# Optimization experiments

Measured on AMD Instinct MI355X. Metric: run time of the kernel, lower is better.

The kernel has to match this reference:

```python
import jax, jax.numpy as jnp
import numpy as np

Z, H, W = 8, 96, 192
WZ, WH, WW = 2, 6, 12
C, HEADS, DEPTH, B = 192, 6, 2, 1
NZ, NH, NW = Z // WZ, H // WH, W // WW
LW = WZ * WH * WW            # 144 tokens per window
WIN_TYPES = NZ * NH          # 64 earth-specific window types
NPOS = WZ * WZ * WH * WH * (2 * WW - 1)  # 3312 relative-position entries
HD = C // HEADS
SCALE = HD ** -0.5
SZ, SH, SW = WZ // 2, WH // 2, WW // 2


def _position_index():
    czi = np.arange(WZ); czj = -np.arange(WZ) * WZ
    chi = np.arange(WH); chj = -np.arange(WH) * WH
    cw = np.arange(WW)
    c1 = np.stack(np.meshgrid(czi, chi, cw, indexing='ij'), 0).reshape(3, -1)
    c2 = np.stack(np.meshgrid(czj, chj, cw, indexing='ij'), 0).reshape(3, -1)
    coords = (c1[:, :, None] - c2[:, None, :]).transpose(1, 2, 0).astype(np.int64).copy()
    coords[:, :, 2] += WW - 1
    coords[:, :, 1] *= 2 * WW - 1
    coords[:, :, 0] *= (2 * WW - 1) * WH * WH
    return coords.sum(-1).reshape(-1)


def _attention_mask():
    m = np.zeros((Z, H, W))
    zs = (slice(0, -WZ), slice(-WZ, -SZ), slice(-SZ, None))
    hs = (slice(0, -WH), slice(-WH, -SH), slice(-SH, None))
    ws = (slice(0, -WW), slice(-WW, -SW), slice(-SW, None))
    cnt = 0
    for z in zs:
        for h in hs:
            for w in ws:
                m[z, h, w] = cnt
                cnt += 1
    mw = m.reshape(NZ, WZ, NH, WH, NW, WW).transpose(0, 2, 4, 1, 3, 5).reshape(-1, LW)
    d = mw[:, None, :] - mw[:, :, None]
    return np.where(d != 0, -100.0, 0.0).astype(np.float32)


def setup_inputs() -> dict:
    key = jax.random.key(0)
    ks = jax.random.split(key, 12)
    s = 0.02
    def rn(k, shape):
        return jax.random.normal(k, shape, jnp.float32) * s
    return {
        'x': jax.random.normal(ks[0], (B, Z * H * W, C), jnp.float32),
        'qkv_w': rn(ks[1], (DEPTH, C, 3 * C)),
        'qkv_b': rn(ks[2], (DEPTH, 3 * C)),
        'proj_w': rn(ks[3], (DEPTH, C, C)),
        'proj_b': rn(ks[4], (DEPTH, C)),
        'bias_tab': rn(ks[5], (DEPTH, NPOS, WIN_TYPES, HEADS)),
        'n1_g': jnp.ones((DEPTH, C), jnp.float32),
        'n1_b': jnp.zeros((DEPTH, C), jnp.float32),
        'n2_g': jnp.ones((DEPTH, C), jnp.float32),
        'n2_b': jnp.zeros((DEPTH, C), jnp.float32),
        'mlp_w1': rn(ks[6], (DEPTH, C, 4 * C)),
        'mlp_b1': rn(ks[7], (DEPTH, 4 * C)),
        'mlp_w2': rn(ks[8], (DEPTH, 4 * C, C)),
        'mlp_b2': rn(ks[9], (DEPTH, C)),
        'pos_index': jnp.asarray(_position_index(), jnp.int32),
        'attn_mask': jnp.asarray(_attention_mask()),
    }


def _ln(x, g, b):
    m = x.mean(-1, keepdims=True)
    v = jnp.mean((x - m) ** 2, -1, keepdims=True)
    return (x - m) / jnp.sqrt(v + 1e-5) * g + b


def _forward(x, qkv_w, qkv_b, proj_w, proj_b, bias_tab, n1_g, n1_b, n2_g, n2_b,
             mlp_w1, mlp_b1, mlp_w2, mlp_b2, pos_index, attn_mask):
    for blk in range(DEPTH):
        roll = (blk % 2 == 1)
        shortcut = x
        h = _ln(x, n1_g[blk], n1_b[blk]).reshape(B, Z, H, W, C)
        if roll:
            h = jnp.roll(h, (-SZ, -SH, -SW), (1, 2, 3))
        # partition windows: (B*nZ*nH*nW, LW, C)
        h = h.reshape(B, NZ, WZ, NH, WH, NW, WW, C).transpose(0, 1, 3, 5, 2, 4, 6, 7).reshape(-1, LW, C)
        B_ = h.shape[0]
        qkv = (h @ qkv_w[blk] + qkv_b[blk]).reshape(B_, LW, 3, HEADS, HD)
        q = qkv[:, :, 0].transpose(0, 2, 1, 3) * SCALE  # (B_, heads, LW, hd)
        k = qkv[:, :, 1].transpose(0, 2, 1, 3)
        v = qkv[:, :, 2].transpose(0, 2, 1, 3)
        attn = jnp.einsum('bhid,bhjd->bhij', q, k)
        # earth-specific bias gathered by relative-position index
        bias = bias_tab[blk][pos_index].reshape(LW, LW, WIN_TYPES, HEADS).transpose(2, 3, 0, 1)
        attn = (attn.reshape(-1, WIN_TYPES, HEADS, LW, LW) + bias).reshape(B_, HEADS, LW, LW)
        if roll:
            attn = (attn.reshape(B, WIN_TYPES * NW, HEADS, LW, LW) + attn_mask[None, :, None]).reshape(B_, HEADS, LW, LW)
        attn = jax.nn.softmax(attn, -1)
        o = jnp.einsum('bhij,bhjd->bhid', attn, v).transpose(0, 2, 1, 3).reshape(B_, LW, C)
        o = o @ proj_w[blk] + proj_b[blk]
        # reverse windows
        o = o.reshape(B, NZ, NH, NW, WZ, WH, WW, C).transpose(0, 1, 4, 2, 5, 3, 6, 7).reshape(B, Z, H, W, C)
        if roll:
            o = jnp.roll(o, (SZ, SH, SW), (1, 2, 3))
        x = shortcut + o.reshape(B, Z * H * W, C)
        h2 = _ln(x, n2_g[blk], n2_b[blk])
        h2 = jax.nn.gelu(h2 @ mlp_w1[blk] + mlp_b1[blk], approximate=False) @ mlp_w2[blk] + mlp_b2[blk]
        x = x + h2
    return x


def reference(x, qkv_w, qkv_b, proj_w, proj_b, bias_tab, n1_g, n1_b, n2_g, n2_b,
              mlp_w1, mlp_b1, mlp_w2, mlp_b2, pos_index, attn_mask):
    return _forward(x, qkv_w, qkv_b, proj_w, proj_b, bias_tab, n1_g, n1_b, n2_g, n2_b,
                    mlp_w1, mlp_b1, mlp_w2, mlp_b2, pos_index, attn_mask)
```

## Files before the change

### kernel.cpp

```cpp
#include <hip/hip_runtime.h>
#include <math.h>

#define TZ 8
#define TH 96
#define TW 192
#define C 192
#define NHEADS 6
#define HDIM 32
#define LW 144
#define NWIN 1024
#define NTOK 147456
#define NPOS 3312
#define QSCALE 0.17677669529663687f

typedef unsigned short u16;
typedef __attribute__((ext_vector_type(8))) short bf8_t;
typedef __attribute__((ext_vector_type(4))) short bf4_t;
typedef __attribute__((ext_vector_type(4))) unsigned short us4_t;
typedef __attribute__((ext_vector_type(4))) float f4_t;

__device__ __forceinline__ float bf2f(u16 u) {
    union { unsigned int i; float f; } c; c.i = ((unsigned int)u) << 16; return c.f;
}
__device__ __forceinline__ u16 f2bf(float f) {
    union { float f; unsigned int i; } c; c.f = f;
    unsigned int x = c.i;
    x += 0x7fffu + ((x >> 16) & 1u);
    return (u16)(x >> 16);
}

__device__ __forceinline__ int win_row_to_token(int r, int roll) {
    int wi = r / LW, l = r % LW;
    int nz = wi >> 8, nh = (wi >> 4) & 15, nw = wi & 15;
    int iz = l / 72, rr = l % 72, ih = rr / 12, iw = rr % 12;
    int z = nz * 2 + iz, h = nh * 6 + ih, w = nw * 12 + iw;
    if (roll) {
        z = (z + 1) & 7;
        h += 3; if (h >= TH) h -= TH;
        w += 6; if (w >= TW) w -= TW;
    }
    return (z * TH + h) * TW + w;
}

__global__ __launch_bounds__(256) void ln_kernel(
    const float* __restrict__ x, const float* __restrict__ g,
    const float* __restrict__ b, u16* __restrict__ xnc,
    int row0, int windowed, int roll)
{
    int wave = threadIdx.x >> 6;
    int lane = threadIdx.x & 63;
    int dl = blockIdx.x * 4 + wave;
    int d = row0 + dl;
    int src = windowed ? win_row_to_token(d, roll) : d;
    const float* xr = x + (size_t)src * C;
    float v0 = xr[lane], v1 = xr[lane + 64], v2 = xr[lane + 128];
    float s = v0 + v1 + v2;
    float sq = v0 * v0 + v1 * v1 + v2 * v2;
    #pragma unroll
    for (int off = 32; off > 0; off >>= 1) {
        s  += __shfl_xor(s, off, 64);
        sq += __shfl_xor(sq, off, 64);
    }
    float mean = s * (1.0f / 192.0f);
    float var  = sq * (1.0f / 192.0f) - mean * mean;
    float rstd = rsqrtf(var + 1e-5f);
    u16* orow = xnc + (size_t)dl * C;
    orow[lane]       = f2bf((v0 - mean) * rstd * g[lane]       + b[lane]);
    orow[lane + 64]  = f2bf((v1 - mean) * rstd * g[lane + 64]  + b[lane + 64]);
    orow[lane + 128] = f2bf((v2 - mean) * rstd * g[lane + 128] + b[lane + 128]);
}

__global__ __launch_bounds__(256) void tconv_kernel(
    const float* __restrict__ W, u16* __restrict__ WT, int K, int N)
{
    int idx = blockIdx.x * 256 + threadIdx.x;
    if (idx >= N * K) return;
    int n = idx / K, k = idx % K;
    WT[idx] = f2bf(W[(size_t)k * N + n]);
}

__global__ __launch_bounds__(256) void biasmat_kernel(
    const float* __restrict__ btab, const int* __restrict__ pidx,
    u16* __restrict__ biasf)
{
    int wt = blockIdx.x, head = blockIdx.y;
    size_t obase = ((size_t)wt * 6 + head) * (LW * LW);
    for (int idx = threadIdx.x; idx < LW * LW; idx += 256) {
        int p = pidx[idx];
        biasf[obase + idx] = f2bf(btab[((size_t)p * 64 + wt) * 6 + head]);
    }
}

template <int MODE>
__global__ __launch_bounds__(256) void mm_kernel(
    const u16* __restrict__ A, const u16* __restrict__ BT,
    const float* __restrict__ bias, void* __restrict__ Cvoid,
    int N, int K, int row0, int roll)
{
    __shared__ alignas(16) u16 As[128 * 72];
    __shared__ alignas(16) u16 Bs[64 * 72];
    int tid = threadIdx.x;
    int mb = blockIdx.y * 128, nb = blockIdx.x * 64;
    int wave = tid >> 6, lane = tid & 63;
    int mh = wave >> 1, nh = wave & 1;
    int lr = lane & 15, g = lane >> 4;

    f4_t acc[4][2];
    #pragma unroll
    for (int mi = 0; mi < 4; mi++)
        #pragma unroll
        for (int ni = 0; ni < 2; ni++)
            acc[mi][ni] = (f4_t){0.f, 0.f, 0.f, 0.f};

    for (int k0 = 0; k0 < K; k0 += 64) {
        #pragma unroll
        for (int it = 0; it < 4; it++) {
            int idx = it * 256 + tid;
            int r = idx >> 3, kc = idx & 7;
            *(bf8_t*)&As[r * 72 + kc * 8] =
                *(const bf8_t*)&A[(size_t)(mb + r) * K + k0 + kc * 8];
        }
        #pragma unroll
        for (int it = 0; it < 2; it++) {
            int idx = it * 256 + tid;
            int r = idx >> 3, kc = idx & 7;
            *(bf8_t*)&Bs[r * 72 + kc * 8] =
                *(const bf8_t*)&BT[(size_t)(nb + r) * K + k0 + kc * 8];
        }
        __syncthreads();
        #pragma unroll
        for (int ks = 0; ks < 2; ks++) {
            bf8_t bfr[2];
            #pragma unroll
            for (int ni = 0; ni < 2; ni++)
                bfr[ni] = *(const bf8_t*)&Bs[(nh * 32 + ni * 16 + lr) * 72 + ks * 32 + g * 8];
            #pragma unroll
            for (int mi = 0; mi < 4; mi++) {
                bf8_t afr = *(const bf8_t*)&As[(mh * 64 + mi * 16 + lr) * 72 + ks * 32 + g * 8];
                #pragma unroll
                for (int ni = 0; ni < 2; ni++)
                    acc[mi][ni] = __builtin_amdgcn_mfma_f32_16x16x32_bf16(
                        afr, bfr[ni], acc[mi][ni], 0, 0, 0);
            }
        }
        __syncthreads();
    }

    #pragma unroll
    for (int mi = 0; mi < 4; mi++) {
        int rbase = mb + mh * 64 + mi * 16 + g * 4;
        int tok[4];
        if (MODE == 1) {
            #pragma unroll
            for (int r = 0; r < 4; r++)
                tok[r] = win_row_to_token(row0 + rbase + r, roll);
        }
        #pragma unroll
        for (int ni = 0; ni < 2; ni++) {
            int col = nb + nh * 32 + ni * 16 + lr;
            float bb = bias[col];
            #pragma unroll
            for (int r = 0; r < 4; r++) {
                float v = acc[mi][ni][r] + bb;
                if (MODE == 0) {
                    if (col < 192) v *= QSCALE;
                    ((u16*)Cvoid)[(size_t)(rbase + r) * 576 + col] = f2bf(v);
                } else if (MODE == 1) {
                    ((float*)Cvoid)[(size_t)tok[r] * C + col] += v;
                } else if (MODE == 2) {
                    v = 0.5f * v * (1.0f + erff(v * 0.70710678118654752f));
                    ((u16*)Cvoid)[(size_t)(rbase + r) * 768 + col] = f2bf(v);
                } else {
                    ((float*)Cvoid)[(size_t)(row0 + rbase + r) * C + col] += v;
                }
            }
        }
    }
}

template <int ROLL>
__global__ __launch_bounds__(192, 4) void attn_kernel(
    const u16* __restrict__ qkvb, const u16* __restrict__ biasf,
    u16* __restrict__ attnb)
{
    __shared__ alignas(16) u16 Qs[144 * 40];
    __shared__ alignas(16) u16 Ks[144 * 40];
    __shared__ alignas(16) u16 Vt[32 * 148];
    __shared__ unsigned char region8[148];

    int bid = blockIdx.x;
    int xcd = bid & 7, slot = bid >> 3;
    int lg = xcd * 768 + slot;
    int wl = lg / 6, head = lg - wl * 6;
    int wt = wl & 63;
    int tid = threadIdx.x;

    const u16* base = qkvb + (size_t)wl * LW * 576;
    for (int c = tid; c < 576; c += 192) {
        int l = c >> 2, d8 = (c & 3) << 3;
        const u16* row = base + (size_t)l * 576 + head * 32;
        *(bf8_t*)&Qs[l * 40 + d8] = *(const bf8_t*)&row[d8];
        *(bf8_t*)&Ks[l * 40 + d8] = *(const bf8_t*)&row[192 + d8];
        bf8_t v8 = *(const bf8_t*)&row[384 + d8];
        #pragma unroll
        for (int m = 0; m < 8; m++)
            Vt[(d8 + m) * 148 + l] = (u16)v8[m];
    }
    bool doMask = false;
    if (ROLL) {
        int nz = wl >> 8, nh = (wl >> 4) & 15, nw = wl & 15;
        doMask = (nz == 3) || (nh == 15) || (nw == 15);
        if (tid < 144) {
            int iz = tid / 72, rr = tid % 72, ih = rr / 12, iw = rr % 12;
            int z = nz * 2 + iz, h = nh * 6 + ih, w = nw * 12 + iw;
            int rz = (z < 6) ? 0 : ((z < 7) ? 1 : 2);
            int rh = (h < 90) ? 0 : ((h < 93) ? 1 : 2);
            int rw2 = (w < 180) ? 0 : ((w < 186) ? 1 : 2);
            region8[tid] = (unsigned char)(rz * 9 + rh * 3 + rw2);
        }
    }
    __syncthreads();

    int wave = tid >> 6, lane = tid & 63;
    int lr = lane & 15, g = lane >> 4;
    int jb = g << 2;
    const f4_t z4 = {0.f, 0.f, 0.f, 0.f};

    for (int itl = 0; itl < 3; itl++) {
        int it = wave * 3 + itl;
        int i_row = it * 16 + lr;
        bf8_t qf = *(const bf8_t*)&Qs[i_row * 40 + (g << 3)];
        f4_t s[9];
        #pragma unroll
        for (int jt = 0; jt < 9; jt++) {
            bf8_t kf = *(const bf8_t*)&Ks[(jt * 16 + lr) * 40 + (g << 3)];
            s[jt] = __builtin_amdgcn_mfma_f32_16x16x32_bf16(kf, qf, z4, 0, 0, 0);
        }

        const u16* bb = biasf + ((size_t)(wt * 6 + head) * LW + i_row) * LW;
        float m4[4] = {-1e30f, -1e30f, -1e30f, -1e30f};
        if (ROLL && doMask) {
            unsigned int ri = region8[i_row];
            #pragma unroll
            for (int jt = 0; jt < 9; jt++) {
                us4_t b4 = *(const us4_t*)&bb[jt * 16 + jb];
                unsigned int rj = *(const unsigned int*)&region8[jt * 16 + jb];
                #pragma unroll
                for (int r = 0; r < 4; r++) {
                    float v = s[jt][r] + bf2f(b4[r]);
                    if (((rj >> (8 * r)) & 255u) != ri) v -= 100.0f;
                    s[jt][r] = v;
                    m4[r] = fmaxf(m4[r], v);
                }
            }
        } else {
            #pragma unroll
            for (int jt = 0; jt < 9; jt++) {
                us4_t b4 = *(const us4_t*)&bb[jt * 16 + jb];
                #pragma unroll
                for (int r = 0; r < 4; r++) {
                    float v = s[jt][r] + bf2f(b4[r]);
                    s[jt][r] = v;
                    m4[r] = fmaxf(m4[r], v);
                }
            }
        }
        float m = fmaxf(fmaxf(m4[0], m4[1]), fmaxf(m4[2], m4[3]));
        m = fmaxf(m, __shfl_xor(m, 16, 64));
        m = fmaxf(m, __shfl_xor(m, 32, 64));

        float l4[4] = {0.f, 0.f, 0.f, 0.f};
        #pragma unroll
        for (int jt = 0; jt < 9; jt++)
            #pragma unroll
            for (int r = 0; r < 4; r++) {
                float p = __expf(s[jt][r] - m);
                s[jt][r] = p;
                l4[r] += p;
            }
        float lsum = (l4[0] + l4[1]) + (l4[2] + l4[3]);
        lsum += __shfl_xor(lsum, 16, 64);
        lsum += __shfl_xor(lsum, 32, 64);
        float inv = 1.0f / lsum;

        bf8_t pfrag[5];
        #pragma unroll
        for (int t = 0; t < 4; t++)
            #pragma unroll
            for (int m2 = 0; m2 < 4; m2++) {
                pfrag[t][m2]     = (short)f2bf(s[2 * t][m2] * inv);
                pfrag[t][4 + m2] = (short)f2bf(s[2 * t + 1][m2] * inv);
            }
        #pragma unroll
        for (int m2 = 0; m2 < 4; m2++) {
            pfrag[4][m2]     = (short)f2bf(s[8][m2] * inv);
            pfrag[4][4 + m2] = 0;
        }

        #pragma unroll
        for (int dt = 0; dt < 2; dt++) {
            const u16* vrow = &Vt[(dt * 16 + lr) * 148];
            f4_t acc = z4;
            #pragma unroll
            for (int t = 0; t < 5; t++) {
                bf4_t va = *(const bf4_t*)&vrow[t * 32 + jb];
                bf8_t af;
                #pragma unroll
                for (int m2 = 0; m2 < 4; m2++) af[m2] = va[m2];
                if (t < 4) {
                    bf4_t vb = *(const bf4_t*)&vrow[t * 32 + 16 + jb];
                    #pragma unroll
                    for (int m2 = 0; m2 < 4; m2++) af[4 + m2] = vb[m2];
                } else {
                    #pragma unroll
                    for (int m2 = 0; m2 < 4; m2++) af[4 + m2] = 0;
                }
                acc = __builtin_amdgcn_mfma_f32_16x16x32_bf16(af, pfrag[t], acc, 0, 0, 0);
            }
            us4_t o;
            #pragma unroll
            for (int r = 0; r < 4; r++) o[r] = f2bf(acc[r]);
            *(us4_t*)&attnb[((size_t)wl * LW + i_row) * 192 + head * 32 + dt * 16 + jb] = o;
        }
    }
}

extern "C" void kernel_launch(void* const* d_in, const int* in_sizes, int n_in,
                              void* d_out, int out_size, void* d_ws, size_t ws_size,
                              hipStream_t stream)
{
    (void)in_sizes; (void)n_in; (void)out_size; (void)ws_size;
    const float* x_in   = (const float*)d_in[0];
    const float* qkv_w  = (const float*)d_in[1];
    const float* qkv_b  = (const float*)d_in[2];
    const float* proj_w = (const float*)d_in[3];
    const float* proj_b = (const float*)d_in[4];
    const float* btab   = (const float*)d_in[5];
    const float* n1g    = (const float*)d_in[6];
    const float* n1b    = (const float*)d_in[7];
    const float* n2g    = (const float*)d_in[8];
    const float* n2b    = (const float*)d_in[9];
    const float* w1     = (const float*)d_in[10];
    const float* b1     = (const float*)d_in[11];
    const float* w2     = (const float*)d_in[12];
    const float* b2     = (const float*)d_in[13];
    const int*   pidx   = (const int*)d_in[14];

    float* x   = (float*)d_out;
    u16* biasf = (u16*)d_ws;
    u16* wT    = biasf + (size_t)64 * 6 * LW * LW;
    u16* xnc   = wT + 884736;
    u16* qkvb  = xnc + (size_t)NTOK * C;
    u16* attnb = qkvb + (size_t)NTOK * 576;
    u16* hidb  = qkvb;

    const size_t WBLK = 442368;
    const size_t OQKV = 0, OPROJ = 110592, OW1 = 147456, OW2 = 294912;

    hipMemcpyAsync(x, x_in, (size_t)NTOK * C * sizeof(float),
                   hipMemcpyDeviceToDevice, stream);

    for (int blk = 0; blk < 2; blk++) {
        u16* wb = wT + blk * WBLK;
        tconv_kernel<<<(576 * 192 + 255) / 256, 256, 0, stream>>>(
            qkv_w + (size_t)blk * C * 576, wb + OQKV, C, 576);
        tconv_kernel<<<(192 * 192 + 255) / 256, 256, 0, stream>>>(
            proj_w + (size_t)blk * C * C, wb + OPROJ, C, 192);
        tconv_kernel<<<(768 * 192 + 255) / 256, 256, 0, stream>>>(
            w1 + (size_t)blk * C * 768, wb + OW1, C, 768);
        tconv_kernel<<<(192 * 768 + 255) / 256, 256, 0, stream>>>(
            w2 + (size_t)blk * 768 * C, wb + OW2, 768, 192);
    }

    for (int blk = 0; blk < 2; blk++) {
        int roll = blk & 1;
        u16* wb = wT + blk * WBLK;
        biasmat_kernel<<<dim3(64, 6), 256, 0, stream>>>(
            btab + (size_t)blk * NPOS * 64 * 6, pidx, biasf);
        ln_kernel<<<NTOK / 4, 256, 0, stream>>>(
            x, n1g + blk * C, n1b + blk * C, xnc, 0, 1, roll);
        mm_kernel<0><<<dim3(9, NTOK / 128), 256, 0, stream>>>(
            xnc, wb + OQKV, qkv_b + blk * 576, qkvb, 576, C, 0, roll);
        if (roll)
            attn_kernel<1><<<NWIN * NHEADS, 192, 0, stream>>>(qkvb, biasf, attnb);
        else
            attn_kernel<0><<<NWIN * NHEADS, 192, 0, stream>>>(qkvb, biasf, attnb);
        mm_kernel<1><<<dim3(3, NTOK / 128), 256, 0, stream>>>(
            attnb, wb + OPROJ, proj_b + blk * C, x, 192, C, 0, roll);
        ln_kernel<<<NTOK / 4, 256, 0, stream>>>(
            x, n2g + blk * C, n2b + blk * C, xnc, 0, 0, 0);
        mm_kernel<2><<<dim3(12, NTOK / 128), 256, 0, stream>>>(
            xnc, wb + OW1, b1 + blk * 768, hidb, 768, C, 0, 0);
        mm_kernel<3><<<dim3(3, NTOK / 128), 256, 0, stream>>>(
            hidb, wb + OW2, b2 + blk * C, x, 192, 768, 0, 0);
    }
}
```

Before: 1.690 ms.

## Widen GEMM tiles to 128x128 with direct global-to-LDS loads

The bf16 MFMA GEMM moves from 128x64 to 128x128 block tiles, so each wave computes a 64x64 sub-tile with 16 accumulators. Tiles are now loaded straight from global memory into LDS with global_load_lds and an unpadded 64-element row stride, which raises reuse per LDS load and removes the register round-trip. The attention kernel also drops its XCD-aware block swizzle in favour of a plain 2D (window, head) grid. In exchange, the unpadded LDS layout may cause bank conflicts on fragment reads. Column counts of 576 and 192 no longer divide the tile, which wastes MFMA work, and the B tile can read weight rows past N.

Measured after the change: 2.127 ms. +25.8%, slower.

```diff
diff --git a/kernel.cpp b/kernel.cpp
--- a/kernel.cpp
+++ b/kernel.cpp
@@ -45,12 +45,11 @@
 __global__ __launch_bounds__(256) void ln_kernel(
     const float* __restrict__ x, const float* __restrict__ g,
     const float* __restrict__ b, u16* __restrict__ xnc,
-    int row0, int windowed, int roll)
+    int windowed, int roll)
 {
     int wave = threadIdx.x >> 6;
     int lane = threadIdx.x & 63;
-    int dl = blockIdx.x * 4 + wave;
-    int d = row0 + dl;
+    int d = blockIdx.x * 4 + wave;
     int src = windowed ? win_row_to_token(d, roll) : d;
     const float* xr = x + (size_t)src * C;
     float v0 = xr[lane], v1 = xr[lane + 64], v2 = xr[lane + 128];
@@ -64,7 +63,7 @@
     float mean = s * (1.0f / 192.0f);
     float var  = sq * (1.0f / 192.0f) - mean * mean;
     float rstd = rsqrtf(var + 1e-5f);
-    u16* orow = xnc + (size_t)dl * C;
+    u16* orow = xnc + (size_t)d * C;
     orow[lane]       = f2bf((v0 - mean) * rstd * g[lane]       + b[lane]);
     orow[lane + 64]  = f2bf((v1 - mean) * rstd * g[lane + 64]  + b[lane + 64]);
     orow[lane + 128] = f2bf((v2 - mean) * rstd * g[lane + 128] + b[lane + 128]);
@@ -95,21 +94,21 @@
 __global__ __launch_bounds__(256) void mm_kernel(
     const u16* __restrict__ A, const u16* __restrict__ BT,
     const float* __restrict__ bias, void* __restrict__ Cvoid,
-    int N, int K, int row0, int roll)
-{
-    __shared__ alignas(16) u16 As[128 * 72];
-    __shared__ alignas(16) u16 Bs[64 * 72];
+    int N, int K, int roll)
+{
+    __shared__ alignas(16) u16 As[128 * 64];
+    __shared__ alignas(16) u16 Bs[128 * 64];
     int tid = threadIdx.x;
-    int mb = blockIdx.y * 128, nb = blockIdx.x * 64;
+    int mb = blockIdx.y * 128, nb = blockIdx.x * 128;
     int wave = tid >> 6, lane = tid & 63;
     int mh = wave >> 1, nh = wave & 1;
     int lr = lane & 15, g = lane >> 4;
 
-    f4_t acc[4][2];
+    f4_t acc[4][4];
     #pragma unroll
     for (int mi = 0; mi < 4; mi++)
         #pragma unroll
-        for (int ni = 0; ni < 2; ni++)
+        for (int ni = 0; ni < 4; ni++)
             acc[mi][ni] = (f4_t){0.f, 0.f, 0.f, 0.f};
 
     for (int k0 = 0; k0 < K; k0 += 64) {
@@ -117,31 +116,40 @@
         for (int it = 0; it < 4; it++) {
             int idx = it * 256 + tid;
             int r = idx >> 3, kc = idx & 7;
-            *(bf8_t*)&As[r * 72 + kc * 8] =
-                *(const bf8_t*)&A[(size_t)(mb + r) * K + k0 + kc * 8];
-        }
-        #pragma unroll
-        for (int it = 0; it < 2; it++) {
+            __builtin_amdgcn_global_load_lds(
+                (const __attribute__((address_space(1))) unsigned int*)
+                    &A[(size_t)(mb + r) * K + k0 + kc * 8],
+                (__attribute__((address_space(3))) unsigned int*)
+                    &As[(size_t)(it * 256 + wave * 64) * 8],
+                16, 0, 0);
+        }
+        #pragma unroll
+        for (int it = 0; it < 4; it++) {
             int idx = it * 256 + tid;
             int r = idx >> 3, kc = idx & 7;
-            *(bf8_t*)&Bs[r * 72 + kc * 8] =
-                *(const bf8_t*)&BT[(size_t)(nb + r) * K + k0 + kc * 8];
+            __builtin_amdgcn_global_load_lds(
+                (const __attribute__((address_space(1))) unsigned int*)
+                    &BT[(size_t)(nb + r) * K + k0 + kc * 8],
+                (__attribute__((address_space(3))) unsigned int*)
+                    &Bs[(size_t)(it * 256 + wave * 64) * 8],
+                16, 0, 0);
         }
         __syncthreads();
         #pragma unroll
         for (int ks = 0; ks < 2; ks++) {
-            bf8_t bfr[2];
-            #pragma unroll
-            for (int ni = 0; ni < 2; ni++)
-                bfr[ni] = *(const bf8_t*)&Bs[(nh * 32 + ni * 16 + lr) * 72 + ks * 32 + g * 8];
-            #pragma unroll
-            for (int mi = 0; mi < 4; mi++) {
-                bf8_t afr = *(const bf8_t*)&As[(mh * 64 + mi * 16 + lr) * 72 + ks * 32 + g * 8];
+            bf8_t bfr[4], afr[4];
+            #pragma unroll
+            for (int ni = 0; ni < 4; ni++)
+                bfr[ni] = *(const bf8_t*)&Bs[(nh * 64 + ni * 16 + lr) * 64 + ks * 32 + g * 8];
+            #pragma unroll
+            for (int mi = 0; mi < 4; mi++)
+                afr[mi] = *(const bf8_t*)&As[(mh * 64 + mi * 16 + lr) * 64 + ks * 32 + g * 8];
+            #pragma unroll
+            for (int mi = 0; mi < 4; mi++)
                 #pragma unroll
-                for (int ni = 0; ni < 2; ni++)
+                for (int ni = 0; ni < 4; ni++)
                     acc[mi][ni] = __builtin_amdgcn_mfma_f32_16x16x32_bf16(
-                        afr, bfr[ni], acc[mi][ni], 0, 0, 0);
-            }
+                        afr[mi], bfr[ni], acc[mi][ni], 0, 0, 0);
         }
         __syncthreads();
     }
@@ -153,25 +161,27 @@
         if (MODE == 1) {
             #pragma unroll
             for (int r = 0; r < 4; r++)
-                tok[r] = win_row_to_token(row0 + rbase + r, roll);
-        }
-        #pragma unroll
-        for (int ni = 0; ni < 2; ni++) {
-            int col = nb + nh * 32 + ni * 16 + lr;
-            float bb = bias[col];
-            #pragma unroll
-            for (int r = 0; r < 4; r++) {
-                float v = acc[mi][ni][r] + bb;
-                if (MODE == 0) {
-                    if (col < 192) v *= QSCALE;
-                    ((u16*)Cvoid)[(size_t)(rbase + r) * 576 + col] = f2bf(v);
-                } else if (MODE == 1) {
-                    ((float*)Cvoid)[(size_t)tok[r] * C + col] += v;
-                } else if (MODE == 2) {
-                    v = 0.5f * v * (1.0f + erff(v * 0.70710678118654752f));
-                    ((u16*)Cvoid)[(size_t)(rbase + r) * 768 + col] = f2bf(v);
-                } else {
-                    ((float*)Cvoid)[(size_t)(row0 + rbase + r) * C + col] += v;
+                tok[r] = win_row_to_token(rbase + r, roll);
+        }
+        #pragma unroll
+        for (int ni = 0; ni < 4; ni++) {
+            int col = nb + nh * 64 + ni * 16 + lr;
+            if (col < N) {
+                float bb = bias[col];
+                #pragma unroll
+                for (int r = 0; r < 4; r++) {
+                    float v = acc[mi][ni][r] + bb;
+                    if (MODE == 0) {
+                        if (col < 192) v *= QSCALE;
+                        ((u16*)Cvoid)[(size_t)(rbase + r) * 576 + col] = f2bf(v);
+                    } else if (MODE == 1) {
+                        ((float*)Cvoid)[(size_t)tok[r] * C + col] += v;
+                    } else if (MODE == 2) {
+                        v = 0.5f * v * (1.0f + erff(v * 0.70710678118654752f));
+                        ((u16*)Cvoid)[(size_t)(rbase + r) * 768 + col] = f2bf(v);
+                    } else {
+                        ((float*)Cvoid)[(size_t)(rbase + r) * C + col] += v;
+                    }
                 }
             }
         }
@@ -188,10 +198,7 @@
     __shared__ alignas(16) u16 Vt[32 * 148];
     __shared__ unsigned char region8[148];
 
-    int bid = blockIdx.x;
-    int xcd = bid & 7, slot = bid >> 3;
-    int lg = xcd * 768 + slot;
-    int wl = lg / 6, head = lg - wl * 6;
+    int wl = blockIdx.x, head = blockIdx.y;
     int wt = wl & 63;
     int tid = threadIdx.x;
 
@@ -378,20 +385,20 @@
         biasmat_kernel<<<dim3(64, 6), 256, 0, stream>>>(
             btab + (size_t)blk * NPOS * 64 * 6, pidx, biasf);
         ln_kernel<<<NTOK / 4, 256, 0, stream>>>(
-            x, n1g + blk * C, n1b + blk * C, xnc, 0, 1, roll);
-        mm_kernel<0><<<dim3(9, NTOK / 128), 256, 0, stream>>>(
-            xnc, wb + OQKV, qkv_b + blk * 576, qkvb, 576, C, 0, roll);
+            x, n1g + blk * C, n1b + blk * C, xnc, 1, roll);
+        mm_kernel<0><<<dim3(5, NTOK / 128), 256, 0, stream>>>(
+            xnc, wb + OQKV, qkv_b + blk * 576, qkvb, 576, C, roll);
         if (roll)
-            attn_kernel<1><<<NWIN * NHEADS, 192, 0, stream>>>(qkvb, biasf, attnb);
+            attn_kernel<1><<<dim3(NWIN, NHEADS), 192, 0, stream>>>(qkvb, biasf, attnb);
         else
-            attn_kernel<0><<<NWIN * NHEADS, 192, 0, stream>>>(qkvb, biasf, attnb);
-        mm_kernel<1><<<dim3(3, NTOK / 128), 256, 0, stream>>>(
-            attnb, wb + OPROJ, proj_b + blk * C, x, 192, C, 0, roll);
+            attn_kernel<0><<<dim3(NWIN, NHEADS), 192, 0, stream>>>(qkvb, biasf, attnb);
+        mm_kernel<1><<<dim3(2, NTOK / 128), 256, 0, stream>>>(
+            attnb, wb + OPROJ, proj_b + blk * C, x, 192, C, roll);
         ln_kernel<<<NTOK / 4, 256, 0, stream>>>(
-            x, n2g + blk * C, n2b + blk * C, xnc, 0, 0, 0);
-        mm_kernel<2><<<dim3(12, NTOK / 128), 256, 0, stream>>>(
-            xnc, wb + OW1, b1 + blk * 768, hidb, 768, C, 0, 0);
-        mm_kernel<3><<<dim3(3, NTOK / 128), 256, 0, stream>>>(
-            hidb, wb + OW2, b2 + blk * C, x, 192, 768, 0, 0);
-    }
-}
+            x, n2g + blk * C, n2b + blk * C, xnc, 0, 0);
+        mm_kernel<2><<<dim3(6, NTOK / 128), 256, 0, stream>>>(
+            xnc, wb + OW1, b1 + blk * 768, hidb, 768, C, 0);
+        mm_kernel<3><<<dim3(2, NTOK / 128), 256, 0, stream>>>(
+            hidb, wb + OW2, b2 + blk * C, x, 192, 768, 0);
+    }
+}
```
